# Optimization experiments

Measured on AMD Instinct MI355X. Metric: run time of the kernel, lower is better.

The kernel has to match this reference:

```python
import jax, jax.numpy as jnp
import numpy as np

T, H, W = 4, 16, 16
S = T * H * W          # 1024 flattened sequence length
C = 576                # embd_dim
NH = 8                 # n_head
DK = C // NH           # 72 per-head dim
L = 4                  # n_layer
B = 4                  # batch
PD = C // 3            # 192 per-axis pos-embed dim


def setup_inputs() -> dict:
    key = jax.random.key(0)
    ks = jax.random.split(key, 10)
    s = 1.0 / np.sqrt(C)
    return {
        "x": jax.random.normal(ks[0], (B, T, H, W, C), jnp.float32),
        "pos0": jax.random.normal(ks[1], (T, PD), jnp.float32) * 0.01,
        "pos1": jax.random.normal(ks[2], (H, PD), jnp.float32) * 0.01,
        "pos2": jax.random.normal(ks[3], (W, PD), jnp.float32) * 0.01,
        "ln1_g": jnp.ones((L, C), jnp.float32),
        "ln1_b": jnp.zeros((L, C), jnp.float32),
        "wq": jax.random.normal(ks[4], (L, C, C), jnp.float32) * s,
        "wk": jax.random.normal(ks[5], (L, C, C), jnp.float32) * s,
        "wv": jax.random.normal(ks[6], (L, C, C), jnp.float32) * s,
        "wo": jax.random.normal(ks[7], (L, C, C), jnp.float32) * (s / np.sqrt(L)),
        "wo_b": jnp.zeros((L, C), jnp.float32),
        "ln2_g": jnp.ones((L, C), jnp.float32),
        "ln2_b": jnp.zeros((L, C), jnp.float32),
        "w1": jax.random.normal(ks[8], (L, C, 4 * C), jnp.float32) * s,
        "b1": jnp.zeros((L, 4 * C), jnp.float32),
        "w2": jax.random.normal(ks[9], (L, 4 * C, C), jnp.float32) * (s / 2.0),
        "b2": jnp.zeros((L, C), jnp.float32),
    }


def _layernorm(x, g, b):
    # Faithful to the source: float32 math, and (1e-5 + rsqrt(var)) multiplier
    # (note: source adds eps to rsqrt, not to var -- replicated exactly).
    xf = x.astype(jnp.float32)
    mu = xf.mean(-1, keepdims=True)
    var = jnp.mean(jnp.square(xf - mu), -1, keepdims=True)
    y = (xf - mu) * (1e-5 + jax.lax.rsqrt(var)) * g + b
    return y.astype(x.dtype)


def _stack(x, pos0, pos1, pos2, ln1_g, ln1_b, wq, wk, wv, wo, wo_b,
           ln2_g, ln2_b, w1, b1, w2, b2):
    b = x.shape[0]
    xf = x.reshape(b, S, C)
    # right_shift (decode_step=None): shift flattened tokens right by one
    xf = jnp.pad(xf[:, :-1], ((0, 0), (1, 0), (0, 0)))
    # broadcast positional embedding, concat along channel
    pos = jnp.concatenate([
        jnp.broadcast_to(pos0[:, None, None, :], (T, H, W, PD)),
        jnp.broadcast_to(pos1[None, :, None, :], (T, H, W, PD)),
        jnp.broadcast_to(pos2[None, None, :, :], (T, H, W, PD)),
    ], axis=-1).reshape(S, C)
    xf = xf + pos

    causal = jnp.tril(jnp.ones((S, S), bool))
    scale = 1.0 / np.sqrt(DK)
    neg_inf = jnp.float32(-jnp.inf)

    for l in range(L):  # fixed small layer loop
        # --- causal full self-attention ---
        h = _layernorm(xf, ln1_g[l], ln1_b[l])
        q = (h @ wq[l]).reshape(b, S, NH, DK).transpose(0, 2, 1, 3)
        k = (h @ wk[l]).reshape(b, S, NH, DK).transpose(0, 2, 1, 3)
        v = (h @ wv[l]).reshape(b, S, NH, DK).transpose(0, 2, 1, 3)
        att = jnp.einsum('bhqd,bhkd->bhqk', q, k) * scale
        att = jnp.where(causal, att, neg_inf)
        att = jax.nn.softmax(att, axis=-1)
        a = jnp.einsum('bhqk,bhkd->bhqd', att, v)
        a = a.transpose(0, 2, 1, 3).reshape(b, S, C)
        xf = xf + a @ wo[l] + wo_b[l]
        # --- FFN with GeLU2: sigmoid(1.702*x)*x ---
        h = _layernorm(xf, ln2_g[l], ln2_b[l])
        h = h @ w1[l] + b1[l]
        h = jax.nn.sigmoid(1.702 * h) * h
        xf = xf + h @ w2[l] + b2[l]
    return xf.reshape(b, T, H, W, C)


def reference(x, pos0, pos1, pos2, ln1_g, ln1_b, wq, wk, wv, wo, wo_b,
              ln2_g, ln2_b, w1, b1, w2, b2):
    return _stack(x, pos0, pos1, pos2, ln1_g, ln1_b, wq, wk, wv, wo, wo_b,
                  ln2_g, ln2_b, w1, b1, w2, b2)
```

## Files before the change

kernel.cpp:

```cpp
#include <hip/hip_runtime.h>
#include <hip/hip_bf16.h>

typedef __hip_bfloat16 bf16;
using bf16x8 = __attribute__((ext_vector_type(8))) short;
using f32x4  = __attribute__((ext_vector_type(4))) float;

#define S_LEN 1024
#define CDIM  576
#define NHEAD 8
#define DKH   72
#define BATCH 4
#define MROWS 4096
#define FFDIM 2304
#define QKVN  1728
#define QKVS  1792

__device__ __forceinline__ void gload16(const void* g, void* l) {
  __builtin_amdgcn_global_load_lds(
      (const __attribute__((address_space(1))) unsigned int*)g,
      (__attribute__((address_space(3))) unsigned int*)l, 16, 0, 0);
}

__device__ __forceinline__ short f2bf_bits(float x) {
  unsigned int u = __float_as_uint(x);
  u += 0x7fffu + ((u >> 16) & 1u);
  return (short)(u >> 16);
}

__global__ __launch_bounds__(256) void transpose_cvt(
    const float* __restrict__ in, bf16* __restrict__ out, int K, int N,
    size_t in_ls, size_t out_ls) {
  __shared__ float tile[32][33];
  const float* inl = in + (size_t)blockIdx.z * in_ls;
  bf16* outl = out + (size_t)blockIdx.z * out_ls;
  int n0 = blockIdx.x * 32, k0 = blockIdx.y * 32;
  int tx = threadIdx.x & 31, ty = threadIdx.x >> 5;
#pragma unroll
  for (int i = 0; i < 32; i += 8)
    tile[ty + i][tx] = inl[(size_t)(k0 + ty + i) * N + (n0 + tx)];
  __syncthreads();
#pragma unroll
  for (int i = 0; i < 32; i += 8)
    outl[(size_t)(n0 + ty + i) * K + (k0 + tx)] = __float2bfloat16(tile[tx][ty + i]);
}

__global__ __launch_bounds__(256) void build_xf(
    const float* __restrict__ x, const float* __restrict__ p0,
    const float* __restrict__ p1, const float* __restrict__ p2,
    float* __restrict__ xf) {
  int idx = blockIdx.x * 256 + threadIdx.x;
  int c4 = idx % 144;
  int s  = (idx / 144) & (S_LEN - 1);
  int b  = idx / (144 * S_LEN);
  int c  = c4 * 4;
  int t = s >> 8, hh = (s >> 4) & 15, w = s & 15;
  float4 pv;
  if (c < 192)       pv = *(const float4*)&p0[t  * 192 + c];
  else if (c < 384)  pv = *(const float4*)&p1[hh * 192 + c - 192];
  else               pv = *(const float4*)&p2[w  * 192 + c - 384];
  float4 xv = make_float4(0.f, 0.f, 0.f, 0.f);
  if (s > 0) xv = *(const float4*)&x[((size_t)b * S_LEN + s - 1) * CDIM + c];
  float4 r = make_float4(xv.x + pv.x, xv.y + pv.y, xv.z + pv.z, xv.w + pv.w);
  *(float4*)&xf[((size_t)b * S_LEN + s) * CDIM + c] = r;
}

__global__ __launch_bounds__(256) void ln_kernel(
    const float* __restrict__ x, const float* __restrict__ g,
    const float* __restrict__ b, bf16* __restrict__ out) {
  int row  = blockIdx.x * 4 + (threadIdx.x >> 6);
  int lane = threadIdx.x & 63;
  const float* xr = x + (size_t)row * CDIM;
  float vals[9];
  float sum = 0.f;
#pragma unroll
  for (int i = 0; i < 9; i++) { vals[i] = xr[lane + 64 * i]; sum += vals[i]; }
#pragma unroll
  for (int o = 1; o < 64; o <<= 1) sum += __shfl_xor(sum, o);
  float mu = sum * (1.f / CDIM);
  float vs = 0.f;
#pragma unroll
  for (int i = 0; i < 9; i++) { float d = vals[i] - mu; vs += d * d; }
#pragma unroll
  for (int o = 1; o < 64; o <<= 1) vs += __shfl_xor(vs, o);
  float mult = 1e-5f + rsqrtf(vs * (1.f / CDIM));
  bf16* orow = out + (size_t)row * CDIM;
#pragma unroll
  for (int i = 0; i < 9; i++) {
    int c = lane + 64 * i;
    orow[c] = __float2bfloat16((vals[i] - mu) * mult * g[c] + b[c]);
  }
}

template <int BM, int BN, bool BIAS, bool RES, int ACT, bool OUTBF>
__global__ __launch_bounds__(256) void gemm3(
    const bf16* __restrict__ A, const bf16* __restrict__ Bt,
    const float* __restrict__ bias, const float* __restrict__ res,
    void* __restrict__ outp, int N, int K) {
  constexpr int MI = BM / 32;
  constexpr int NI = BN / 32;
  constexpr int AJ = BM / 64;
  constexpr int BJ = BN / 64;
  __shared__ __align__(16) short ldsA[BM * 32];
  __shared__ __align__(16) short ldsB[BN * 32];
  const int tid = threadIdx.x, lane = tid & 63, wave = tid >> 6;
  const int lr = lane & 15, quad = lane >> 4;
  const int m0 = blockIdx.x * BM, n0 = blockIdx.y * BN;
  const int wm = (wave & 1) * (BM / 2), wn = (wave >> 1) * (BN / 2);
  f32x4 acc[MI][NI] = {};

  const int srow = lane >> 2, scol = (lane & 3) * 8;
  const short* Ag[AJ];
  short* ldsAw[AJ];
#pragma unroll
  for (int j = 0; j < AJ; j++) {
    Ag[j] = (const short*)A + (size_t)(m0 + (wave * AJ + j) * 16 + srow) * K + scol;
    ldsAw[j] = &ldsA[(wave * AJ + j) * 512];
  }
  const short* Bg[BJ];
  short* ldsBw[BJ];
#pragma unroll
  for (int j = 0; j < BJ; j++) {
    Bg[j] = (const short*)Bt + (size_t)(n0 + (wave * BJ + j) * 16 + srow) * K + scol;
    ldsBw[j] = &ldsB[(wave * BJ + j) * 512];
  }

  for (int k0 = 0; k0 < K; k0 += 32) {
#pragma unroll
    for (int j = 0; j < AJ; j++) gload16(Ag[j] + k0, ldsAw[j]);
#pragma unroll
    for (int j = 0; j < BJ; j++) gload16(Bg[j] + k0, ldsBw[j]);
    __syncthreads();
    bf16x8 af[MI], bfv[NI];
#pragma unroll
    for (int mi = 0; mi < MI; mi++)
      af[mi] = *(const bf16x8*)&ldsA[(wm + mi * 16 + lr) * 32 + quad * 8];
#pragma unroll
    for (int ni = 0; ni < NI; ni++)
      bfv[ni] = *(const bf16x8*)&ldsB[(wn + ni * 16 + lr) * 32 + quad * 8];
#pragma unroll
    for (int mi = 0; mi < MI; mi++)
#pragma unroll
      for (int ni = 0; ni < NI; ni++)
        acc[mi][ni] = __builtin_amdgcn_mfma_f32_16x16x32_bf16(af[mi], bfv[ni], acc[mi][ni], 0, 0, 0);
    __syncthreads();
  }

  float* fout = (float*)outp;
  bf16*  bout = (bf16*)outp;
#pragma unroll
  for (int mi = 0; mi < MI; mi++)
#pragma unroll
    for (int ni = 0; ni < NI; ni++) {
      int col = n0 + wn + ni * 16 + lr;
#pragma unroll
      for (int r = 0; r < 4; r++) {
        int row = m0 + wm + mi * 16 + quad * 4 + r;
        float v = acc[mi][ni][r];
        if (BIAS) v += bias[col];
        if (ACT == 1) v = v / (1.f + __expf(-1.702f * v));
        size_t idx = (size_t)row * N + col;
        if (RES) v += res[idx];
        if (OUTBF) bout[idx] = __float2bfloat16(v);
        else       fout[idx] = v;
      }
    }
}

__global__ __launch_bounds__(256) void attn_mfma(
    const bf16* __restrict__ qkv, bf16* __restrict__ a) {
  __shared__ short ldsK[12 * 512];
  __shared__ short ldsVt[80][104];
  __shared__ short ldsP[4 * 1024];
  const int bh = blockIdx.y, b = bh >> 3, h = bh & 7;
  const int tid = threadIdx.x, wave = tid >> 6, lane = tid & 63;
  const int lr = lane & 15, quad = lane >> 4;
  const int qt = 15 - (int)blockIdx.x;
  const float scale = 0.11785113019775793f;
  const int qcol = h * DKH, kcol = CDIM + h * DKH, vcol = 2 * CDIM + h * DKH;

  const int qrow = qt * 64 + wave * 16 + lr;
  const short* qg = (const short*)qkv + (size_t)(b * S_LEN + qrow) * QKVS + qcol;
  bf16x8 qfrag[3];
#pragma unroll
  for (int c = 0; c < 3; c++) {
    int d0 = c * 32 + quad * 8;
    bf16x8 z = {0, 0, 0, 0, 0, 0, 0, 0};
    qfrag[c] = (d0 < DKH) ? *(const bf16x8*)(qg + d0) : z;
  }
  f32x4 oacc[5] = {};
  float m[4], l[4];
#pragma unroll
  for (int r = 0; r < 4; r++) { m[r] = -1e30f; l[r] = 0.f; }

  for (int kt = 0; kt <= qt; kt++) {
    __syncthreads();
    {
      const short* kg = (const short*)qkv +
          (size_t)(b * S_LEN + kt * 64 + wave * 16 + lr) * QKVS + kcol + quad * 8;
#pragma unroll
      for (int c = 0; c < 3; c++)
        gload16(kg + c * 32, &ldsK[(wave * 3 + c) * 512]);
    }
    {
      int key = tid & 63, dgb = tid >> 6;
      const short* vg = (const short*)qkv + (size_t)(b * S_LEN + kt * 64 + key) * QKVS + vcol;
#pragma unroll
      for (int pass = 0; pass < 3; pass++) {
        int d0 = (dgb + pass * 4) * 8;
        if (d0 < 80) {
          bf16x8 vv = {0, 0, 0, 0, 0, 0, 0, 0};
          if (d0 < DKH) vv = *(const bf16x8*)(vg + d0);
#pragma unroll
          for (int j = 0; j < 8; j++) ldsVt[d0 + j][key] = vv[j];
        }
      }
    }
    __syncthreads();
    f32x4 sacc[4] = {};
#pragma unroll
    for (int nc = 0; nc < 4; nc++)
#pragma unroll
      for (int c = 0; c < 3; c++) {
        bf16x8 kf = *(const bf16x8*)&ldsK[(nc * 3 + c) * 512 + lane * 8];
        sacc[nc] = __builtin_amdgcn_mfma_f32_16x16x32_bf16(qfrag[c], kf, sacc[nc], 0, 0, 0);
      }
    float tmax[4];
#pragma unroll
    for (int r = 0; r < 4; r++) tmax[r] = -1e30f;
    bool diag = (kt == qt);
#pragma unroll
    for (int nc = 0; nc < 4; nc++)
#pragma unroll
      for (int r = 0; r < 4; r++) {
        float s = sacc[nc][r] * scale;
        if (diag && (nc * 16 + lr > wave * 16 + quad * 4 + r)) s = -1e30f;
        sacc[nc][r] = s;
        tmax[r] = fmaxf(tmax[r], s);
      }
#pragma unroll
    for (int r = 0; r < 4; r++) {
      tmax[r] = fmaxf(tmax[r], __shfl_xor(tmax[r], 1));
      tmax[r] = fmaxf(tmax[r], __shfl_xor(tmax[r], 2));
      tmax[r] = fmaxf(tmax[r], __shfl_xor(tmax[r], 4));
      tmax[r] = fmaxf(tmax[r], __shfl_xor(tmax[r], 8));
    }
    float alpha[4], psum[4];
#pragma unroll
    for (int r = 0; r < 4; r++) {
      float mn = fmaxf(m[r], tmax[r]);
      alpha[r] = __expf(m[r] - mn);
      m[r] = mn;
      psum[r] = 0.f;
    }
#pragma unroll
    for (int nc = 0; nc < 4; nc++)
#pragma unroll
      for (int r = 0; r < 4; r++) {
        float p = __expf(sacc[nc][r] - m[r]);
        psum[r] += p;
        int col = nc * 16 + lr;
        ldsP[wave * 1024 + (col >> 5) * 512 +
             (((col >> 3) & 3) * 16 + quad * 4 + r) * 8 + (col & 7)] = f2bf_bits(p);
      }
#pragma unroll
    for (int r = 0; r < 4; r++) {
      psum[r] += __shfl_xor(psum[r], 1);
      psum[r] += __shfl_xor(psum[r], 2);
      psum[r] += __shfl_xor(psum[r], 4);
      psum[r] += __shfl_xor(psum[r], 8);
      l[r] = l[r] * alpha[r] + psum[r];
    }
#pragma unroll
    for (int dc = 0; dc < 5; dc++)
#pragma unroll
      for (int r = 0; r < 4; r++) oacc[dc][r] *= alpha[r];
    __builtin_amdgcn_sched_barrier(0);
    bf16x8 pfrag[2];
#pragma unroll
    for (int kc = 0; kc < 2; kc++)
      pfrag[kc] = *(const bf16x8*)&ldsP[wave * 1024 + kc * 512 + lane * 8];
#pragma unroll
    for (int dc = 0; dc < 5; dc++)
#pragma unroll
      for (int kc = 0; kc < 2; kc++) {
        bf16x8 vf = *(const bf16x8*)&ldsVt[dc * 16 + lr][kc * 32 + quad * 8];
        oacc[dc] = __builtin_amdgcn_mfma_f32_16x16x32_bf16(pfrag[kc], vf, oacc[dc], 0, 0, 0);
      }
  }

#pragma unroll
  for (int dc = 0; dc < 5; dc++) {
    int d = dc * 16 + lr;
    if (d < DKH) {
#pragma unroll
      for (int r = 0; r < 4; r++) {
        int row = qt * 64 + wave * 16 + quad * 4 + r;
        float val = oacc[dc][r] / l[r];
        a[(size_t)(b * S_LEN + row) * CDIM + h * DKH + d] = __float2bfloat16(val);
      }
    }
  }
}

extern "C" void kernel_launch(void* const* d_in, const int* in_sizes, int n_in,
                              void* d_out, int out_size, void* d_ws, size_t ws_size,
                              hipStream_t stream) {
  const float* x    = (const float*)d_in[0];
  const float* pos0 = (const float*)d_in[1];
  const float* pos1 = (const float*)d_in[2];
  const float* pos2 = (const float*)d_in[3];
  const float* ln1g = (const float*)d_in[4];
  const float* ln1b = (const float*)d_in[5];
  const float* wq   = (const float*)d_in[6];
  const float* wk   = (const float*)d_in[7];
  const float* wv   = (const float*)d_in[8];
  const float* wo   = (const float*)d_in[9];
  const float* wob  = (const float*)d_in[10];
  const float* ln2g = (const float*)d_in[11];
  const float* ln2b = (const float*)d_in[12];
  const float* w1   = (const float*)d_in[13];
  const float* b1   = (const float*)d_in[14];
  const float* w2   = (const float*)d_in[15];
  const float* b2   = (const float*)d_in[16];

  char* ws = (char*)d_ws;
  size_t off = 0;
  auto alloc = [&](size_t bytes) {
    char* p = ws + off;
    off += (bytes + 255) & ~(size_t)255;
    return p;
  };
  bf16* wqkvT = (bf16*)alloc((size_t)4 * QKVS * CDIM * sizeof(bf16));
  bf16* woT   = (bf16*)alloc((size_t)4 * CDIM * CDIM * sizeof(bf16));
  bf16* w1T   = (bf16*)alloc((size_t)4 * FFDIM * CDIM * sizeof(bf16));
  bf16* w2T   = (bf16*)alloc((size_t)4 * CDIM * FFDIM * sizeof(bf16));
  bf16* hbuf  = (bf16*)alloc((size_t)MROWS * CDIM * sizeof(bf16));
  bf16* abuf  = (bf16*)alloc((size_t)MROWS * CDIM * sizeof(bf16));
  bf16* ubuf  = (bf16*)alloc((size_t)MROWS * FFDIM * sizeof(bf16));
  bf16* qkvb  = (bf16*)alloc((size_t)MROWS * QKVS * sizeof(bf16));
  float* xf   = (float*)d_out;

  const size_t ils  = (size_t)CDIM * CDIM;
  const size_t ils2 = (size_t)CDIM * FFDIM;
  const size_t qkv_ls = (size_t)QKVS * CDIM;
  transpose_cvt<<<dim3(18, 18, 4), 256, 0, stream>>>(wq, wqkvT, CDIM, CDIM, ils, qkv_ls);
  transpose_cvt<<<dim3(18, 18, 4), 256, 0, stream>>>(wk, wqkvT + (size_t)CDIM * CDIM, CDIM, CDIM, ils, qkv_ls);
  transpose_cvt<<<dim3(18, 18, 4), 256, 0, stream>>>(wv, wqkvT + (size_t)2 * CDIM * CDIM, CDIM, CDIM, ils, qkv_ls);
  transpose_cvt<<<dim3(18, 18, 4), 256, 0, stream>>>(wo, woT, CDIM, CDIM, ils, ils);
  transpose_cvt<<<dim3(72, 18, 4), 256, 0, stream>>>(w1, w1T, CDIM, FFDIM, ils2, ils2);
  transpose_cvt<<<dim3(18, 72, 4), 256, 0, stream>>>(w2, w2T, FFDIM, CDIM, ils2, ils2);

  build_xf<<<2304, 256, 0, stream>>>(x, pos0, pos1, pos2, xf);

  for (int l = 0; l < 4; l++) {
    bf16* wqkv_l = wqkvT + (size_t)l * qkv_ls;
    bf16* wo_l   = woT   + (size_t)l * ils;
    bf16* w1_l   = w1T   + (size_t)l * ils2;
    bf16* w2_l   = w2T   + (size_t)l * ils2;

    ln_kernel<<<1024, 256, 0, stream>>>(xf, ln1g + l * CDIM, ln1b + l * CDIM, hbuf);
    gemm3<128, 128, false, false, 0, true><<<dim3(32, QKVS / 128), 256, 0, stream>>>(
        hbuf, wqkv_l, nullptr, nullptr, qkvb, QKVS, CDIM);
    attn_mfma<<<dim3(16, 32), 256, 0, stream>>>(qkvb, abuf);
    gemm3<128, 64, true, true, 0, false><<<dim3(32, CDIM / 64), 256, 0, stream>>>(
        abuf, wo_l, wob + l * CDIM, xf, xf, CDIM, CDIM);
    ln_kernel<<<1024, 256, 0, stream>>>(xf, ln2g + l * CDIM, ln2b + l * CDIM, hbuf);
    gemm3<128, 128, true, false, 1, true><<<dim3(32, FFDIM / 128), 256, 0, stream>>>(
        hbuf, w1_l, b1 + l * FFDIM, nullptr, ubuf, FFDIM, CDIM);
    gemm3<128, 64, true, true, 0, false><<<dim3(32, CDIM / 64), 256, 0, stream>>>(
        ubuf, w2_l, b2 + l * CDIM, xf, xf, CDIM, FFDIM);
  }
}
```

Baseline: 815.7 us.

## Double-buffer attention K/V tiles, drop QKV padding, retune GEMM tile sizes

The attention kernel now double-buffers K and V tiles in LDS. It prefetches the next key tile (K via global_load_lds, V into registers) while computing the current one, leaving one barrier per iteration. The QKV buffer drops its padding to 1728 columns, and the third K chunk (dims 64-71) is loaded by a single wave into a compact region. GEMM tiles shrink (128x64 for QKV and FFN1, 64x64 for the output projections) to launch more blocks on the many-CU device, at the cost of less per-block reuse and more LDS in attention.

```diff
diff --git a/kernel.cpp b/kernel.cpp
--- a/kernel.cpp
+++ b/kernel.cpp
@@ -13,7 +13,6 @@
 #define MROWS 4096
 #define FFDIM 2304
 #define QKVN  1728
-#define QKVS  1792
 
 __device__ __forceinline__ void gload16(const void* g, void* l) {
   __builtin_amdgcn_global_load_lds(
@@ -168,9 +167,9 @@
 
 __global__ __launch_bounds__(256) void attn_mfma(
     const bf16* __restrict__ qkv, bf16* __restrict__ a) {
-  __shared__ short ldsK[12 * 512];
-  __shared__ short ldsVt[80][104];
-  __shared__ short ldsP[4 * 1024];
+  __shared__ __align__(16) short ldsK[2][9 * 512];
+  __shared__ __align__(16) short ldsVt[2][80][104];
+  __shared__ __align__(16) short ldsP[4 * 1024];
   const int bh = blockIdx.y, b = bh >> 3, h = bh & 7;
   const int tid = threadIdx.x, wave = tid >> 6, lane = tid & 63;
   const int lr = lane & 15, quad = lane >> 4;
@@ -179,7 +178,7 @@
   const int qcol = h * DKH, kcol = CDIM + h * DKH, vcol = 2 * CDIM + h * DKH;
 
   const int qrow = qt * 64 + wave * 16 + lr;
-  const short* qg = (const short*)qkv + (size_t)(b * S_LEN + qrow) * QKVS + qcol;
+  const short* qg = (const short*)qkv + (size_t)(b * S_LEN + qrow) * QKVN + qcol;
   bf16x8 qfrag[3];
 #pragma unroll
   for (int c = 0; c < 3; c++) {
@@ -192,38 +191,58 @@
 #pragma unroll
   for (int r = 0; r < 4; r++) { m[r] = -1e30f; l[r] = 0.f; }
 
+  const size_t ktstep = (size_t)64 * QKVN;
+  const short* kg0 = (const short*)qkv + (size_t)(b * S_LEN + wave * 16 + lr) * QKVN + kcol + quad * 8;
+  const short* kg2 = (const short*)qkv + (size_t)(b * S_LEN + lane) * QKVN + kcol + 64;
+  const int vkey = tid & 63, vdgb = tid >> 6;
+  const short* vg0 = (const short*)qkv + (size_t)(b * S_LEN + vkey) * QKVN + vcol;
+
+  {
+#pragma unroll
+    for (int c = 0; c < 2; c++)
+      gload16(kg0 + c * 32, &ldsK[0][(wave * 2 + c) * 512]);
+    if (wave == 0) gload16(kg2, &ldsK[0][8 * 512]);
+#pragma unroll
+    for (int pass = 0; pass < 3; pass++) {
+      int d0 = (vdgb + pass * 4) * 8;
+      if (d0 < 80) {
+        bf16x8 vv = {0, 0, 0, 0, 0, 0, 0, 0};
+        if (d0 < DKH) vv = *(const bf16x8*)(vg0 + d0);
+#pragma unroll
+        for (int j = 0; j < 8; j++) ldsVt[0][d0 + j][vkey] = vv[j];
+      }
+    }
+  }
+  __syncthreads();
+
   for (int kt = 0; kt <= qt; kt++) {
-    __syncthreads();
-    {
-      const short* kg = (const short*)qkv +
-          (size_t)(b * S_LEN + kt * 64 + wave * 16 + lr) * QKVS + kcol + quad * 8;
-#pragma unroll
-      for (int c = 0; c < 3; c++)
-        gload16(kg + c * 32, &ldsK[(wave * 3 + c) * 512]);
-    }
-    {
-      int key = tid & 63, dgb = tid >> 6;
-      const short* vg = (const short*)qkv + (size_t)(b * S_LEN + kt * 64 + key) * QKVS + vcol;
+    const int cur = kt & 1, nxt = cur ^ 1;
+    const bool pf = (kt < qt);
+    bf16x8 vpre[3];
+    if (pf) {
+      const short* kg = kg0 + (size_t)(kt + 1) * ktstep;
+#pragma unroll
+      for (int c = 0; c < 2; c++)
+        gload16(kg + c * 32, &ldsK[nxt][(wave * 2 + c) * 512]);
+      if (wave == 0) gload16(kg2 + (size_t)(kt + 1) * ktstep, &ldsK[nxt][8 * 512]);
+      const short* vg = vg0 + (size_t)(kt + 1) * ktstep;
 #pragma unroll
       for (int pass = 0; pass < 3; pass++) {
-        int d0 = (dgb + pass * 4) * 8;
-        if (d0 < 80) {
-          bf16x8 vv = {0, 0, 0, 0, 0, 0, 0, 0};
-          if (d0 < DKH) vv = *(const bf16x8*)(vg + d0);
-#pragma unroll
-          for (int j = 0; j < 8; j++) ldsVt[d0 + j][key] = vv[j];
-        }
-      }
-    }
-    __syncthreads();
+        int d0 = (vdgb + pass * 4) * 8;
+        bf16x8 z = {0, 0, 0, 0, 0, 0, 0, 0};
+        vpre[pass] = (d0 < DKH) ? *(const bf16x8*)(vg + d0) : z;
+      }
+    }
     f32x4 sacc[4] = {};
 #pragma unroll
-    for (int nc = 0; nc < 4; nc++)
-#pragma unroll
-      for (int c = 0; c < 3; c++) {
-        bf16x8 kf = *(const bf16x8*)&ldsK[(nc * 3 + c) * 512 + lane * 8];
-        sacc[nc] = __builtin_amdgcn_mfma_f32_16x16x32_bf16(qfrag[c], kf, sacc[nc], 0, 0, 0);
-      }
+    for (int nc = 0; nc < 4; nc++) {
+      bf16x8 kf0 = *(const bf16x8*)&ldsK[cur][(nc * 2 + 0) * 512 + lane * 8];
+      sacc[nc] = __builtin_amdgcn_mfma_f32_16x16x32_bf16(qfrag[0], kf0, sacc[nc], 0, 0, 0);
+      bf16x8 kf1 = *(const bf16x8*)&ldsK[cur][(nc * 2 + 1) * 512 + lane * 8];
+      sacc[nc] = __builtin_amdgcn_mfma_f32_16x16x32_bf16(qfrag[1], kf1, sacc[nc], 0, 0, 0);
+      bf16x8 kf2 = *(const bf16x8*)&ldsK[cur][8 * 512 + (nc * 16 + lr) * 8];
+      sacc[nc] = __builtin_amdgcn_mfma_f32_16x16x32_bf16(qfrag[2], kf2, sacc[nc], 0, 0, 0);
+    }
     float tmax[4];
 #pragma unroll
     for (int r = 0; r < 4; r++) tmax[r] = -1e30f;
@@ -283,9 +302,20 @@
     for (int dc = 0; dc < 5; dc++)
 #pragma unroll
       for (int kc = 0; kc < 2; kc++) {
-        bf16x8 vf = *(const bf16x8*)&ldsVt[dc * 16 + lr][kc * 32 + quad * 8];
+        bf16x8 vf = *(const bf16x8*)&ldsVt[cur][dc * 16 + lr][kc * 32 + quad * 8];
         oacc[dc] = __builtin_amdgcn_mfma_f32_16x16x32_bf16(pfrag[kc], vf, oacc[dc], 0, 0, 0);
       }
+    if (pf) {
+#pragma unroll
+      for (int pass = 0; pass < 3; pass++) {
+        int d0 = (vdgb + pass * 4) * 8;
+        if (d0 < 80) {
+#pragma unroll
+          for (int j = 0; j < 8; j++) ldsVt[nxt][d0 + j][vkey] = vpre[pass][j];
+        }
+      }
+    }
+    __syncthreads();
   }
 
 #pragma unroll
@@ -330,19 +360,19 @@
     off += (bytes + 255) & ~(size_t)255;
     return p;
   };
-  bf16* wqkvT = (bf16*)alloc((size_t)4 * QKVS * CDIM * sizeof(bf16));
+  bf16* wqkvT = (bf16*)alloc((size_t)4 * QKVN * CDIM * sizeof(bf16));
   bf16* woT   = (bf16*)alloc((size_t)4 * CDIM * CDIM * sizeof(bf16));
   bf16* w1T   = (bf16*)alloc((size_t)4 * FFDIM * CDIM * sizeof(bf16));
   bf16* w2T   = (bf16*)alloc((size_t)4 * CDIM * FFDIM * sizeof(bf16));
   bf16* hbuf  = (bf16*)alloc((size_t)MROWS * CDIM * sizeof(bf16));
   bf16* abuf  = (bf16*)alloc((size_t)MROWS * CDIM * sizeof(bf16));
   bf16* ubuf  = (bf16*)alloc((size_t)MROWS * FFDIM * sizeof(bf16));
-  bf16* qkvb  = (bf16*)alloc((size_t)MROWS * QKVS * sizeof(bf16));
+  bf16* qkvb  = (bf16*)alloc((size_t)MROWS * QKVN * sizeof(bf16));
   float* xf   = (float*)d_out;
 
   const size_t ils  = (size_t)CDIM * CDIM;
   const size_t ils2 = (size_t)CDIM * FFDIM;
-  const size_t qkv_ls = (size_t)QKVS * CDIM;
+  const size_t qkv_ls = (size_t)QKVN * CDIM;
   transpose_cvt<<<dim3(18, 18, 4), 256, 0, stream>>>(wq, wqkvT, CDIM, CDIM, ils, qkv_ls);
   transpose_cvt<<<dim3(18, 18, 4), 256, 0, stream>>>(wk, wqkvT + (size_t)CDIM * CDIM, CDIM, CDIM, ils, qkv_ls);
   transpose_cvt<<<dim3(18, 18, 4), 256, 0, stream>>>(wv, wqkvT + (size_t)2 * CDIM * CDIM, CDIM, CDIM, ils, qkv_ls);
@@ -359,15 +389,15 @@
     bf16* w2_l   = w2T   + (size_t)l * ils2;
 
     ln_kernel<<<1024, 256, 0, stream>>>(xf, ln1g + l * CDIM, ln1b + l * CDIM, hbuf);
-    gemm3<128, 128, false, false, 0, true><<<dim3(32, QKVS / 128), 256, 0, stream>>>(
-        hbuf, wqkv_l, nullptr, nullptr, qkvb, QKVS, CDIM);
+    gemm3<128, 64, false, false, 0, true><<<dim3(32, QKVN / 64), 256, 0, stream>>>(
+        hbuf, wqkv_l, nullptr, nullptr, qkvb, QKVN, CDIM);
     attn_mfma<<<dim3(16, 32), 256, 0, stream>>>(qkvb, abuf);
-    gemm3<128, 64, true, true, 0, false><<<dim3(32, CDIM / 64), 256, 0, stream>>>(
+    gemm3<64, 64, true, true, 0, false><<<dim3(64, CDIM / 64), 256, 0, stream>>>(
         abuf, wo_l, wob + l * CDIM, xf, xf, CDIM, CDIM);
     ln_kernel<<<1024, 256, 0, stream>>>(xf, ln2g + l * CDIM, ln2b + l * CDIM, hbuf);
-    gemm3<128, 128, true, false, 1, true><<<dim3(32, FFDIM / 128), 256, 0, stream>>>(
+    gemm3<128, 64, true, false, 1, true><<<dim3(32, FFDIM / 64), 256, 0, stream>>>(
         hbuf, w1_l, b1 + l * FFDIM, nullptr, ubuf, FFDIM, CDIM);
-    gemm3<128, 64, true, true, 0, false><<<dim3(32, CDIM / 64), 256, 0, stream>>>(
+    gemm3<64, 64, true, true, 0, false><<<dim3(64, CDIM / 64), 256, 0, stream>>>(
         ubuf, w2_l, b2 + l * CDIM, xf, xf, CDIM, FFDIM);
   }
 }
```

Measured after the change: 719.4 us. 11.8% less time.
